# Kernel optimization log

Hardware: AMD Instinct MI355X
Metric: run time of the kernel (lower is better)

## Reference

```python
import jax, jax.numpy as jnp
import numpy as np
from jax import lax

# Constants derived from init_kwargs
VIDEO_FPS = 30
DELTA_T_US = 1000000.0 / VIDEO_FPS
REFRACTORY_US = 0.0
THRESHOLD = 0.0
N_NOISE = 10
T, H, W = 96, 720, 1280
P_NOISE = 0.001


def setup_inputs() -> dict:
    key = jax.random.key(0)
    k1, k2, k3 = jax.random.split(key, 3)
    tensor = jax.random.uniform(k1, (T, H, W), dtype=jnp.float32) * 255.0  # pixel frames
    state = jnp.zeros((H, W), dtype=jnp.float32)
    timesurface = jnp.zeros((H, W), dtype=jnp.float32)
    on_noise = jax.random.uniform(k2, (N_NOISE, H, W)) < P_NOISE
    off_noise = jax.random.uniform(k3, (N_NOISE, H, W)) < P_NOISE
    return {"tensor": tensor, "state": state, "timesurface": timesurface,
            "on_noise": on_noise, "off_noise": off_noise}


def reference(tensor, state, timesurface, on_noise, off_noise):
    def step(carry, i_t):
        st, ts, t_idx = carry
        cnt = t_idx + 1                              # int(t_us // delta_t) == frame count
        t_us = cnt.astype(jnp.float32) * DELTA_T_US
        min_time = jnp.floor((t_us - REFRACTORY_US) / DELTA_T_US)
        idle = ts <= min_time                        # (H, W) bool
        diff = (i_t - st) * idle
        on = diff > THRESHOLD
        off = diff < THRESHOLD
        zero = jnp.abs(diff) <= THRESHOLD
        non_zero = ~zero
        out = jnp.where(zero, 127.0, jnp.where(on, 255.0, jnp.where(off, 0.0, diff)))
        new_st = jnp.where(non_zero, i_t, st)
        new_ts = jnp.where(non_zero, cnt.astype(ts.dtype), ts)
        n_on = jnp.take(on_noise, cnt % N_NOISE, axis=0)
        n_off = jnp.take(off_noise, cnt % N_NOISE, axis=0)
        out = jnp.where(n_off, 0.0, jnp.where(n_on, 255.0, out))
        return (new_st, new_ts, t_idx + 1), out

    init = (state, timesurface, jnp.int32(0))
    _, diffs = lax.scan(step, init, tensor)
    return diffs  # (T, H, W)
```

## Files before the change

### kernel.cpp

```cpp
#include <hip/hip_runtime.h>

constexpr int T_FRAMES = 96;
constexpr int HH = 720;
constexpr int WW = 1280;
constexpr int HW = HH * WW;
constexpr int N_NOISE = 10;

constexpr int TC  = 4;
constexpr int TPC = T_FRAMES / TC;
constexpr int PIX = 4;
constexpr int BLOCK = 256;

constexpr int DET_BLOCKS = 64;

__global__ __launch_bounds__(BLOCK)
void detect_noise_dtype(const uint4* __restrict__ noise,
                        unsigned int* __restrict__ counters) {
    const int i = blockIdx.x * BLOCK + threadIdx.x;
    const uint4 v = noise[i];
    unsigned a = 0, b = 0;
    const unsigned w[4] = {v.x, v.y, v.z, v.w};
#pragma unroll
    for (int k = 0; k < 4; ++k) {
        a += ((w[k] & 0x000000ffu) != 0);
        b += ((w[k] & 0x0000ff00u) != 0);
        b += ((w[k] & 0x00ff0000u) != 0);
        b += ((w[k] & 0xff000000u) != 0);
    }
    if (a) atomicAdd(&counters[0], a);
    if (b) atomicAdd(&counters[1], b);
}

template <int FLAG>
__device__ __forceinline__ uint4 load_noise4(const void* __restrict__ p, int idx) {
    if (FLAG == 1) {
        const uchar4 v = *reinterpret_cast<const uchar4*>(
            reinterpret_cast<const unsigned char*>(p) + idx);
        return make_uint4(v.x, v.y, v.z, v.w);
    } else if (FLAG == 0) {
        const int4 v = *reinterpret_cast<const int4*>(
            reinterpret_cast<const int*>(p) + idx);
        return make_uint4(v.x != 0, v.y != 0, v.z != 0, v.w != 0);
    } else {
        const float4 v = *reinterpret_cast<const float4*>(
            reinterpret_cast<const float*>(p) + idx);
        return make_uint4(v.x != 0.f, v.y != 0.f, v.z != 0.f, v.w != 0.f);
    }
}

__device__ __forceinline__ float classify(float cur, float prev,
                                          unsigned on, unsigned off) {
    const float d = cur - prev;
    float o = (d == 0.f) ? 127.f : (d > 0.f ? 255.f : 0.f);
    if (on)  o = 255.f;
    if (off) o = 0.f;
    return o;
}

template <int FLAG>
__device__ void neuro_body(const float* __restrict__ tensor,
                           const float* __restrict__ state,
                           const void* __restrict__ on_noise,
                           const void* __restrict__ off_noise,
                           float* __restrict__ out) {
    const int p = (blockIdx.x * BLOCK + threadIdx.x) * PIX;
    if (p >= HW) return;
    const int t0 = blockIdx.y * TPC;

    float4 prev;
    if (t0 == 0) {
        prev = *reinterpret_cast<const float4*>(state + p);
    } else {
        prev = *reinterpret_cast<const float4*>(tensor + (t0 - 1) * HW + p);
    }

#pragma unroll 4
    for (int t = t0; t < t0 + TPC; ++t) {
        const float4 cur = *reinterpret_cast<const float4*>(tensor + t * HW + p);
        const int ni = (t + 1) % N_NOISE;
        const uint4 n_on  = load_noise4<FLAG>(on_noise,  ni * HW + p);
        const uint4 n_off = load_noise4<FLAG>(off_noise, ni * HW + p);

        float4 o;
        o.x = classify(cur.x, prev.x, n_on.x, n_off.x);
        o.y = classify(cur.y, prev.y, n_on.y, n_off.y);
        o.z = classify(cur.z, prev.z, n_on.z, n_off.z);
        o.w = classify(cur.w, prev.w, n_on.w, n_off.w);

        *reinterpret_cast<float4*>(out + t * HW + p) = o;
        prev = cur;
    }
}

__global__ __launch_bounds__(BLOCK)
void neuro_kernel(const float* __restrict__ tensor,
                  const float* __restrict__ state,
                  const void* __restrict__ on_noise,
                  const void* __restrict__ off_noise,
                  float* __restrict__ out,
                  const unsigned int* __restrict__ counters) {
    const unsigned a = counters[0], b = counters[1];
    const int flag = (b == 0u) ? 0 : ((a == 0u) ? 2 : 1);
    if (flag == 1)      neuro_body<1>(tensor, state, on_noise, off_noise, out);
    else if (flag == 0) neuro_body<0>(tensor, state, on_noise, off_noise, out);
    else                neuro_body<2>(tensor, state, on_noise, off_noise, out);
}

extern "C" void kernel_launch(void* const* d_in, const int* in_sizes, int n_in,
                              void* d_out, int out_size, void* d_ws, size_t ws_size,
                              hipStream_t stream) {
    const float* tensor   = (const float*)d_in[0];
    const float* state    = (const float*)d_in[1];
    const void*  on_noise  = d_in[3];
    const void*  off_noise = d_in[4];
    float* out = (float*)d_out;
    unsigned int* counters = (unsigned int*)d_ws;

    hipMemsetAsync(counters, 0, 2 * sizeof(unsigned int), stream);

    detect_noise_dtype<<<DET_BLOCKS, BLOCK, 0, stream>>>(
        (const uint4*)on_noise, counters);

    dim3 grid(HW / PIX / BLOCK, TC);
    neuro_kernel<<<grid, BLOCK, 0, stream>>>(
        tensor, state, on_noise, off_noise, out, counters);
}
```

Baseline: 707.3 us.

## Preload noise masks into per-thread bitmasks and stream all frames per thread

Each thread now loads all ten on/off noise planes once, packing them into 64-bit bitmasks, then walks all 96 frames for its four pixels. This removes the per-frame noise reloads and the time-chunk split that re-read a boundary frame. Tensor loads and output stores become nontemporal, and the block size drops to 64 with a 1D grid. The catch is less parallelism per pixel (one thread spans every frame) and a long serial loop per thread.

```diff
diff --git a/kernel.cpp b/kernel.cpp
--- a/kernel.cpp
+++ b/kernel.cpp
@@ -6,17 +6,18 @@
 constexpr int HW = HH * WW;
 constexpr int N_NOISE = 10;
 
-constexpr int TC  = 4;
-constexpr int TPC = T_FRAMES / TC;
 constexpr int PIX = 4;
-constexpr int BLOCK = 256;
+constexpr int BLOCK = 64;
+constexpr int NBLOCKS = HW / PIX / BLOCK;
+
+typedef float f4 __attribute__((ext_vector_type(4)));
 
 constexpr int DET_BLOCKS = 64;
 
-__global__ __launch_bounds__(BLOCK)
+__global__ __launch_bounds__(256)
 void detect_noise_dtype(const uint4* __restrict__ noise,
                         unsigned int* __restrict__ counters) {
-    const int i = blockIdx.x * BLOCK + threadIdx.x;
+    const int i = blockIdx.x * 256 + threadIdx.x;
     const uint4 v = noise[i];
     unsigned a = 0, b = 0;
     const unsigned w[4] = {v.x, v.y, v.z, v.w};
@@ -32,19 +33,20 @@
 }
 
 template <int FLAG>
-__device__ __forceinline__ uint4 load_noise4(const void* __restrict__ p, int idx) {
+__device__ __forceinline__ unsigned pack4(const void* __restrict__ p, int idx) {
     if (FLAG == 1) {
         const uchar4 v = *reinterpret_cast<const uchar4*>(
             reinterpret_cast<const unsigned char*>(p) + idx);
-        return make_uint4(v.x, v.y, v.z, v.w);
+        return (v.x ? 1u : 0u) | (v.y ? 2u : 0u) | (v.z ? 4u : 0u) | (v.w ? 8u : 0u);
     } else if (FLAG == 0) {
-        const int4 v = *reinterpret_cast<const int4*>(
-            reinterpret_cast<const int*>(p) + idx);
-        return make_uint4(v.x != 0, v.y != 0, v.z != 0, v.w != 0);
+        const int4 v = *(reinterpret_cast<const int4*>(
+            reinterpret_cast<const int*>(p) + idx));
+        return (v.x ? 1u : 0u) | (v.y ? 2u : 0u) | (v.z ? 4u : 0u) | (v.w ? 8u : 0u);
     } else {
-        const float4 v = *reinterpret_cast<const float4*>(
-            reinterpret_cast<const float*>(p) + idx);
-        return make_uint4(v.x != 0.f, v.y != 0.f, v.z != 0.f, v.w != 0.f);
+        const float4 v = *(reinterpret_cast<const float4*>(
+            reinterpret_cast<const float*>(p) + idx));
+        return (v.x != 0.f ? 1u : 0u) | (v.y != 0.f ? 2u : 0u) |
+               (v.z != 0.f ? 4u : 0u) | (v.w != 0.f ? 8u : 0u);
     }
 }
 
@@ -64,31 +66,36 @@
                            const void* __restrict__ off_noise,
                            float* __restrict__ out) {
     const int p = (blockIdx.x * BLOCK + threadIdx.x) * PIX;
-    if (p >= HW) return;
-    const int t0 = blockIdx.y * TPC;
 
-    float4 prev;
-    if (t0 == 0) {
-        prev = *reinterpret_cast<const float4*>(state + p);
-    } else {
-        prev = *reinterpret_cast<const float4*>(tensor + (t0 - 1) * HW + p);
+    unsigned long long onb = 0, offb = 0;
+#pragma unroll
+    for (int ni = 0; ni < N_NOISE; ++ni) {
+        onb  |= (unsigned long long)pack4<FLAG>(on_noise,  ni * HW + p) << (ni * 4);
+        offb |= (unsigned long long)pack4<FLAG>(off_noise, ni * HW + p) << (ni * 4);
     }
 
-#pragma unroll 4
-    for (int t = t0; t < t0 + TPC; ++t) {
-        const float4 cur = *reinterpret_cast<const float4*>(tensor + t * HW + p);
-        const int ni = (t + 1) % N_NOISE;
-        const uint4 n_on  = load_noise4<FLAG>(on_noise,  ni * HW + p);
-        const uint4 n_off = load_noise4<FLAG>(off_noise, ni * HW + p);
+    f4 prev = *reinterpret_cast<const f4*>(state + p);
+    const float* tp = tensor + p;
+    float*       op = out + p;
 
-        float4 o;
-        o.x = classify(cur.x, prev.x, n_on.x, n_off.x);
-        o.y = classify(cur.y, prev.y, n_on.y, n_off.y);
-        o.z = classify(cur.z, prev.z, n_on.z, n_off.z);
-        o.w = classify(cur.w, prev.w, n_on.w, n_off.w);
+    int ni = 1;
+#pragma unroll 8
+    for (int t = 0; t < T_FRAMES; ++t) {
+        const f4 cur = __builtin_nontemporal_load(reinterpret_cast<const f4*>(tp));
+        const unsigned mon  = (unsigned)(onb  >> (ni * 4)) & 0xFu;
+        const unsigned moff = (unsigned)(offb >> (ni * 4)) & 0xFu;
 
-        *reinterpret_cast<float4*>(out + t * HW + p) = o;
+        f4 o;
+        o.x = classify(cur.x, prev.x, mon & 1u, moff & 1u);
+        o.y = classify(cur.y, prev.y, mon & 2u, moff & 2u);
+        o.z = classify(cur.z, prev.z, mon & 4u, moff & 4u);
+        o.w = classify(cur.w, prev.w, mon & 8u, moff & 8u);
+
+        __builtin_nontemporal_store(o, reinterpret_cast<f4*>(op));
         prev = cur;
+        tp += HW;
+        op += HW;
+        ni = (ni == N_NOISE - 1) ? 0 : ni + 1;
     }
 }
 
@@ -118,10 +125,9 @@
 
     hipMemsetAsync(counters, 0, 2 * sizeof(unsigned int), stream);
 
-    detect_noise_dtype<<<DET_BLOCKS, BLOCK, 0, stream>>>(
+    detect_noise_dtype<<<DET_BLOCKS, 256, 0, stream>>>(
         (const uint4*)on_noise, counters);
 
-    dim3 grid(HW / PIX / BLOCK, TC);
-    neuro_kernel<<<grid, BLOCK, 0, stream>>>(
+    neuro_kernel<<<NBLOCKS, BLOCK, 0, stream>>>(
         tensor, state, on_noise, off_noise, out, counters);
 }
```

After: 609.7 us. 1.16x faster.
